# Optimization experiments

Hardware: AMD Instinct MI355X
Metric: run time of the kernel (lower is better)

Reference implementation:

```python
import jax, jax.numpy as jnp
import numpy as np

V = 1_000_000   # sparse_id_num
D = 64          # embedding_dim
F = 26          # sparse_feature_cnt
L = 8           # ids per feature bag (fixed-size ragged regularization)
B = 4096        # batch
IN_DIM = F * D  # 1664
HIDDENS = (1024, 1024, 512)


def setup_inputs() -> dict:
    key = jax.random.key(0)
    ks = jax.random.split(key, 4 + 4 * len(HIDDENS))
    inp = {}
    inp["x"] = jax.random.randint(ks[0], (B, F, L), 0, V, dtype=jnp.int64)
    inp["emb_table"] = jax.random.normal(ks[1], (V, D), dtype=jnp.float32) * 0.01
    ki = 2
    for i, h in enumerate(HIDDENS):
        inp[f"w1_{i}"] = jax.random.normal(ks[ki], (IN_DIM, h), dtype=jnp.float32) * 0.02
        inp[f"b1_{i}"] = jnp.zeros((h,), dtype=jnp.float32)
        inp[f"w2_{i}"] = jax.random.normal(ks[ki + 1], (h, IN_DIM), dtype=jnp.float32) * 0.02
        inp[f"b2_{i}"] = jnp.zeros((IN_DIM,), dtype=jnp.float32)
        ki += 2
    inp["lin_w"] = jax.random.normal(ks[ki], (IN_DIM, 1), dtype=jnp.float32) * 0.02
    inp["lin_b"] = jnp.zeros((1,), dtype=jnp.float32)
    return inp


def reference(x, emb_table,
              w1_0, b1_0, w2_0, b2_0,
              w1_1, b1_1, w2_1, b2_1,
              w1_2, b1_2, w2_2, b2_2,
              lin_w, lin_b):
    # Batched embedding lookup + sum-pool over bag dim + concat over features.
    # x: [B, F, L] -> gather [B, F, L, D] -> sum over L -> [B, F, D] -> [B, F*D]
    pooled = emb_table[x].sum(axis=2)              # [B, F, D]
    feat = pooled.reshape(x.shape[0], -1)          # [B, F*D]
    # Residual blocks: relu(linear2(relu(linear1(x))) + x)
    for w1, b1, w2, b2 in ((w1_0, b1_0, w2_0, b2_0),
                           (w1_1, b1_1, w2_1, b2_1),
                           (w1_2, b1_2, w2_2, b2_2)):
        h = jax.nn.relu(feat @ w1 + b1)
        feat = jax.nn.relu(h @ w2 + b2 + feat)
    return jax.nn.sigmoid(feat @ lin_w + lin_b)    # [B, 1]
```

## Files before the change

### kernel.cpp

```cpp
#include <hip/hip_runtime.h>

#define BATCH 4096
#define FEATS 26
#define BAG   8
#define EDIM  64
#define INDIM 1664

typedef short bf16x8 __attribute__((ext_vector_type(8)));
typedef float f32x4  __attribute__((ext_vector_type(4)));
typedef unsigned short u16x8 __attribute__((ext_vector_type(8)));

__device__ __forceinline__ unsigned short f2bf(float f) {
    unsigned u = __float_as_uint(f);
    unsigned r = (u + 0x7FFFu + ((u >> 16) & 1u)) >> 16;
    return (unsigned short)r;
}
__device__ __forceinline__ float bf2f(unsigned short h) {
    return __uint_as_float((unsigned)h << 16);
}
__device__ __forceinline__ void async_cp16(const void* g, void* lds_base_uniform) {
    __builtin_amdgcn_global_load_lds(
        (const __attribute__((address_space(1))) unsigned int*)g,
        (__attribute__((address_space(3))) unsigned int*)lds_base_uniform,
        16, 0, 0);
}
#define WAITCNT_VM(n) __builtin_amdgcn_s_waitcnt(0x0F70 | (n))

__global__ __launch_bounds__(256) void transpose_all(
    const float* __restrict__ w10, unsigned short* __restrict__ o10,
    const float* __restrict__ w20, unsigned short* __restrict__ o20,
    const float* __restrict__ w11, unsigned short* __restrict__ o11,
    const float* __restrict__ w21, unsigned short* __restrict__ o21,
    const float* __restrict__ w12, unsigned short* __restrict__ o12,
    const float* __restrict__ w22, unsigned short* __restrict__ o22)
{
    const float* in; unsigned short* out; int R, C;
    switch (blockIdx.z) {
        case 0:  in = w10; out = o10; R = INDIM; C = 1024;  break;
        case 1:  in = w20; out = o20; R = 1024;  C = INDIM; break;
        case 2:  in = w11; out = o11; R = INDIM; C = 1024;  break;
        case 3:  in = w21; out = o21; R = 1024;  C = INDIM; break;
        case 4:  in = w12; out = o12; R = INDIM; C = 512;   break;
        default: in = w22; out = o22; R = 512;   C = INDIM; break;
    }
    const int c0 = blockIdx.x * 64, r0 = blockIdx.y * 64;
    if (c0 >= C || r0 >= R) return;

    __shared__ unsigned short tile[64][65];
    const int t = threadIdx.x;
    const int tc = t & 63, tr = t >> 6;
#pragma unroll
    for (int i = 0; i < 16; ++i) {
        int r = tr + i * 4;
        tile[r][tc] = f2bf(in[(long long)(r0 + r) * C + c0 + tc]);
    }
    __syncthreads();
    const int wr = t >> 3, wc = t & 7;
#pragma unroll
    for (int half = 0; half < 2; ++half) {
        int row = wr + half * 32;
        u16x8 v;
#pragma unroll
        for (int j = 0; j < 8; ++j) v[j] = tile[wc * 8 + j][row];
        *(u16x8*)(out + (long long)(c0 + row) * R + r0 + wc * 8) = v;
    }
}

__global__ __launch_bounds__(256) void embed_pool(
    const int* __restrict__ x, const float* __restrict__ emb,
    unsigned short* __restrict__ feat)
{
    int bag  = blockIdx.x * 4 + (threadIdx.x >> 6);
    int lane = threadIdx.x & 63;
    int b = bag / FEATS;
    int f = bag - b * FEATS;
    const int* xs = x + (long long)bag * BAG;
    float s = 0.f;
#pragma unroll
    for (int l = 0; l < BAG; ++l) {
        int id = xs[l];
        s += emb[(long long)id * EDIM + lane];
    }
    feat[(long long)b * INDIM + f * EDIM + lane] = f2bf(s);
}

#define NBUF 4
__global__ __launch_bounds__(512) void gemm_bf16(
    const unsigned short* __restrict__ A, const unsigned short* __restrict__ Wt,
    const float* __restrict__ bias, const unsigned short* __restrict__ res,
    unsigned short* __restrict__ out, int M, int N, int K, int do_relu)
{
    __shared__ unsigned short As[NBUF * 128 * 32];
    __shared__ unsigned short Bs[NBUF * 128 * 32];

    const int t    = threadIdx.x;
    const int nxg = gridDim.x;
    const int lin = blockIdx.y * nxg + blockIdx.x;
    const int q   = (nxg * gridDim.y) >> 3;
    const int tile = (lin & 7) * q + (lin >> 3);
    const int ty  = tile / nxg;
    const int bCol = (tile - ty * nxg) * 128;
    const int bRow = ty * 128;

    const int wave = t >> 6, lane = t & 63;
    const int wm = wave & 1, wn = wave >> 1;
    const int lm = lane & 15, quad = lane >> 4;

    const int srow = lane >> 2;
    const int sq   = (lane & 3) ^ ((lane >> 3) & 3);
    const unsigned short* Ag = A  + (long long)(bRow + wave * 16 + srow) * K + sq * 8;
    const unsigned short* Bg = Wt + (long long)(bCol + wave * 16 + srow) * K + sq * 8;
    unsigned short* AsW = As + wave * 512;
    unsigned short* BsW = Bs + wave * 512;

    const int T = K / 32;
    f32x4 acc[4][2] = {};
    const int slot = (quad ^ ((lm >> 1) & 3)) * 8;

#define ISSUE(tile_)  do { int _b = (tile_) & (NBUF - 1);                         \
        async_cp16(Ag + (long long)(tile_) * 32, AsW + _b * 4096);                \
        async_cp16(Bg + (long long)(tile_) * 32, BsW + _b * 4096); } while (0)

#define COMPUTE(tile_) do { int _b = (tile_) & (NBUF - 1);                        \
        const unsigned short* _a = As + _b * 4096;                                \
        const unsigned short* _bp = Bs + _b * 4096;                               \
        bf16x8 af[4], bf[2];                                                      \
        _Pragma("unroll")                                                         \
        for (int i = 0; i < 4; ++i)                                               \
            af[i] = *(const bf16x8*)&_a[(wm * 64 + i * 16 + lm) * 32 + slot];     \
        _Pragma("unroll")                                                         \
        for (int j = 0; j < 2; ++j)                                               \
            bf[j] = *(const bf16x8*)&_bp[(wn * 32 + j * 16 + lm) * 32 + slot];    \
        _Pragma("unroll")                                                         \
        for (int i = 0; i < 4; ++i)                                               \
            _Pragma("unroll")                                                     \
            for (int j = 0; j < 2; ++j)                                           \
                acc[i][j] = __builtin_amdgcn_mfma_f32_16x16x32_bf16(              \
                    af[i], bf[j], acc[i][j], 0, 0, 0); } while (0)

    ISSUE(0);
    ISSUE(1);
    for (int tt = 0; tt < T - 2; ++tt) {
        ISSUE(tt + 2);
        WAITCNT_VM(4);
        asm volatile("" ::: "memory");
        __builtin_amdgcn_s_barrier();
        asm volatile("" ::: "memory");
        COMPUTE(tt);
    }
    WAITCNT_VM(2);
    asm volatile("" ::: "memory");
    __builtin_amdgcn_s_barrier();
    asm volatile("" ::: "memory");
    COMPUTE(T - 2);
    WAITCNT_VM(0);
    asm volatile("" ::: "memory");
    __builtin_amdgcn_s_barrier();
    asm volatile("" ::: "memory");
    COMPUTE(T - 1);

#pragma unroll
    for (int i = 0; i < 4; ++i) {
#pragma unroll
        for (int j = 0; j < 2; ++j) {
            int col = bCol + wn * 32 + j * 16 + lm;
            float bv = bias[col];
#pragma unroll
            for (int r = 0; r < 4; ++r) {
                int row = bRow + wm * 64 + i * 16 + quad * 4 + r;
                float v = acc[i][j][r] + bv;
                if (res) v += bf2f(res[(long long)row * N + col]);
                if (do_relu) v = fmaxf(v, 0.f);
                out[(long long)row * N + col] = f2bf(v);
            }
        }
    }
#undef ISSUE
#undef COMPUTE
}

__global__ __launch_bounds__(256) void final_head(
    const unsigned short* __restrict__ feat, const float* __restrict__ lin_w,
    const float* __restrict__ lin_b, float* __restrict__ out)
{
    int row  = blockIdx.x * 4 + (threadIdx.x >> 6);
    int lane = threadIdx.x & 63;
    const unsigned short* fr = feat + (long long)row * INDIM;
    float s = 0.f;
#pragma unroll
    for (int it = 0; it < INDIM / 64; ++it)
        s += bf2f(fr[it * 64 + lane]) * lin_w[it * 64 + lane];
#pragma unroll
    for (int off = 32; off; off >>= 1)
        s += __shfl_down(s, off, 64);
    if (lane == 0)
        out[row] = 1.f / (1.f + __expf(-(s + lin_b[0])));
}

extern "C" void kernel_launch(void* const* d_in, const int* in_sizes, int n_in,
                              void* d_out, int out_size, void* d_ws, size_t ws_size,
                              hipStream_t stream) {
    const int*   x    = (const int*)  d_in[0];
    const float* emb  = (const float*)d_in[1];
    const float* w1_0 = (const float*)d_in[2];
    const float* b1_0 = (const float*)d_in[3];
    const float* w2_0 = (const float*)d_in[4];
    const float* b2_0 = (const float*)d_in[5];
    const float* w1_1 = (const float*)d_in[6];
    const float* b1_1 = (const float*)d_in[7];
    const float* w2_1 = (const float*)d_in[8];
    const float* b2_1 = (const float*)d_in[9];
    const float* w1_2 = (const float*)d_in[10];
    const float* b1_2 = (const float*)d_in[11];
    const float* w2_2 = (const float*)d_in[12];
    const float* b2_2 = (const float*)d_in[13];
    const float* linw = (const float*)d_in[14];
    const float* linb = (const float*)d_in[15];
    float* out = (float*)d_out;

    unsigned short* feat = (unsigned short*)d_ws;
    unsigned short* h    = feat + (long long)BATCH * INDIM;
    unsigned short* p    = h + (long long)BATCH * 1024;
    unsigned short* w1_0t = p; p += 1024 * INDIM;
    unsigned short* w2_0t = p; p += INDIM * 1024;
    unsigned short* w1_1t = p; p += 1024 * INDIM;
    unsigned short* w2_1t = p; p += INDIM * 1024;
    unsigned short* w1_2t = p; p += 512 * INDIM;
    unsigned short* w2_2t = p; p += INDIM * 512;

    transpose_all<<<dim3(26, 26, 6), 256, 0, stream>>>(
        w1_0, w1_0t, w2_0, w2_0t, w1_1, w1_1t, w2_1, w2_1t, w1_2, w1_2t, w2_2, w2_2t);

    embed_pool<<<BATCH * FEATS / 4, 256, 0, stream>>>(x, emb, feat);

    gemm_bf16<<<dim3(1024/128, BATCH/128), 512, 0, stream>>>(
        feat, w1_0t, b1_0, nullptr, h, BATCH, 1024, INDIM, 1);
    gemm_bf16<<<dim3(INDIM/128, BATCH/128), 512, 0, stream>>>(
        h, w2_0t, b2_0, feat, feat, BATCH, INDIM, 1024, 1);
    gemm_bf16<<<dim3(1024/128, BATCH/128), 512, 0, stream>>>(
        feat, w1_1t, b1_1, nullptr, h, BATCH, 1024, INDIM, 1);
    gemm_bf16<<<dim3(INDIM/128, BATCH/128), 512, 0, stream>>>(
        h, w2_1t, b2_1, feat, feat, BATCH, INDIM, 1024, 1);
    gemm_bf16<<<dim3(512/128, BATCH/128), 512, 0, stream>>>(
        feat, w1_2t, b1_2, nullptr, h, BATCH, 512, INDIM, 1);
    gemm_bf16<<<dim3(INDIM/128, BATCH/128), 512, 0, stream>>>(
        h, w2_2t, b2_2, feat, feat, BATCH, INDIM, 512, 1);

    final_head<<<BATCH / 4, 256, 0, stream>>>(feat, linw, linb, out);
}
```

Before: 534.7 us.

## Deepen GEMM LDS pipeline, halve barriers, add narrow-tile GEMM and two-bag pooling

The GEMM's LDS ring buffer grows from 4 to 8 stages, and each barrier now covers two K-tiles instead of one, so the kernel synchronises half as often. The GEMM is templated on the N tile width, and the 512-wide layer uses 64-wide tiles so it launches more blocks. In that variant, waves 4-7 redundantly reload the same B rows. The embedding pooling kernel now handles two bags per wave to have more independent gathers in flight. The larger LDS footprint, about 128KB per block, likely limits occupancy to one block per CU.

Measured after the change: 553.4 us. 1.04x slower.

```diff
diff --git a/kernel.cpp b/kernel.cpp
--- a/kernel.cpp
+++ b/kernel.cpp
@@ -70,36 +70,44 @@
     const int* __restrict__ x, const float* __restrict__ emb,
     unsigned short* __restrict__ feat)
 {
-    int bag  = blockIdx.x * 4 + (threadIdx.x >> 6);
-    int lane = threadIdx.x & 63;
-    int b = bag / FEATS;
-    int f = bag - b * FEATS;
-    const int* xs = x + (long long)bag * BAG;
-    float s = 0.f;
+    const int wave = threadIdx.x >> 6, lane = threadIdx.x & 63;
+    const int bag0 = (blockIdx.x * 4 + wave) * 2;
+    const int* xs = x + (long long)bag0 * BAG;
+    float s0 = 0.f, s1 = 0.f;
 #pragma unroll
     for (int l = 0; l < BAG; ++l) {
-        int id = xs[l];
-        s += emb[(long long)id * EDIM + lane];
-    }
-    feat[(long long)b * INDIM + f * EDIM + lane] = f2bf(s);
-}
-
-#define NBUF 4
+        int id0 = xs[l];
+        int id1 = xs[BAG + l];
+        s0 += emb[(long long)id0 * EDIM + lane];
+        s1 += emb[(long long)id1 * EDIM + lane];
+    }
+#pragma unroll
+    for (int g = 0; g < 2; ++g) {
+        int bag = bag0 + g;
+        int b = bag / FEATS, f = bag - b * FEATS;
+        feat[(long long)b * INDIM + f * EDIM + lane] = f2bf(g ? s1 : s0);
+    }
+}
+
+#define NBUF 8
+template<int BN>
 __global__ __launch_bounds__(512) void gemm_bf16(
     const unsigned short* __restrict__ A, const unsigned short* __restrict__ Wt,
     const float* __restrict__ bias, const unsigned short* __restrict__ res,
     unsigned short* __restrict__ out, int M, int N, int K, int do_relu)
 {
+    constexpr int JN = BN / 64;
+
     __shared__ unsigned short As[NBUF * 128 * 32];
-    __shared__ unsigned short Bs[NBUF * 128 * 32];
-
-    const int t    = threadIdx.x;
+    __shared__ unsigned short Bs[NBUF * BN * 32];
+
+    const int t = threadIdx.x;
     const int nxg = gridDim.x;
     const int lin = blockIdx.y * nxg + blockIdx.x;
     const int q   = (nxg * gridDim.y) >> 3;
     const int tile = (lin & 7) * q + (lin >> 3);
     const int ty  = tile / nxg;
-    const int bCol = (tile - ty * nxg) * 128;
+    const int bCol = (tile - ty * nxg) * BN;
     const int bRow = ty * 128;
 
     const int wave = t >> 6, lane = t & 63;
@@ -108,62 +116,68 @@
 
     const int srow = lane >> 2;
     const int sq   = (lane & 3) ^ ((lane >> 3) & 3);
+    const int slot = (quad ^ ((lm >> 1) & 3)) * 8;
+
+    const int bwave = (BN == 128) ? wave : (wave & 3);
     const unsigned short* Ag = A  + (long long)(bRow + wave * 16 + srow) * K + sq * 8;
-    const unsigned short* Bg = Wt + (long long)(bCol + wave * 16 + srow) * K + sq * 8;
+    const unsigned short* Bg = Wt + (long long)(bCol + bwave * 16 + srow) * K + sq * 8;
     unsigned short* AsW = As + wave * 512;
-    unsigned short* BsW = Bs + wave * 512;
+    unsigned short* BsW = Bs + bwave * 512;
 
     const int T = K / 32;
-    f32x4 acc[4][2] = {};
-    const int slot = (quad ^ ((lm >> 1) & 3)) * 8;
+    const int P = T / 2;
+    f32x4 acc[4][JN] = {};
 
 #define ISSUE(tile_)  do { int _b = (tile_) & (NBUF - 1);                         \
         async_cp16(Ag + (long long)(tile_) * 32, AsW + _b * 4096);                \
-        async_cp16(Bg + (long long)(tile_) * 32, BsW + _b * 4096); } while (0)
+        async_cp16(Bg + (long long)(tile_) * 32, BsW + _b * (BN * 32)); } while (0)
 
 #define COMPUTE(tile_) do { int _b = (tile_) & (NBUF - 1);                        \
         const unsigned short* _a = As + _b * 4096;                                \
-        const unsigned short* _bp = Bs + _b * 4096;                               \
-        bf16x8 af[4], bf[2];                                                      \
+        const unsigned short* _bp = Bs + _b * (BN * 32);                          \
+        bf16x8 af[4], bf[JN];                                                     \
         _Pragma("unroll")                                                         \
         for (int i = 0; i < 4; ++i)                                               \
             af[i] = *(const bf16x8*)&_a[(wm * 64 + i * 16 + lm) * 32 + slot];     \
         _Pragma("unroll")                                                         \
-        for (int j = 0; j < 2; ++j)                                               \
-            bf[j] = *(const bf16x8*)&_bp[(wn * 32 + j * 16 + lm) * 32 + slot];    \
+        for (int j = 0; j < JN; ++j)                                              \
+            bf[j] = *(const bf16x8*)&_bp[(wn * (BN / 4) + j * 16 + lm) * 32 + slot]; \
         _Pragma("unroll")                                                         \
         for (int i = 0; i < 4; ++i)                                               \
             _Pragma("unroll")                                                     \
-            for (int j = 0; j < 2; ++j)                                           \
+            for (int j = 0; j < JN; ++j)                                          \
                 acc[i][j] = __builtin_amdgcn_mfma_f32_16x16x32_bf16(              \
                     af[i], bf[j], acc[i][j], 0, 0, 0); } while (0)
 
-    ISSUE(0);
-    ISSUE(1);
-    for (int tt = 0; tt < T - 2; ++tt) {
-        ISSUE(tt + 2);
-        WAITCNT_VM(4);
+    ISSUE(0); ISSUE(1); ISSUE(2); ISSUE(3);
+    for (int p = 0; p < P - 2; ++p) {
+        ISSUE(2 * p + 4);
+        ISSUE(2 * p + 5);
+        WAITCNT_VM(8);
         asm volatile("" ::: "memory");
         __builtin_amdgcn_s_barrier();
         asm volatile("" ::: "memory");
-        COMPUTE(tt);
-    }
-    WAITCNT_VM(2);
+        COMPUTE(2 * p);
+        COMPUTE(2 * p + 1);
+    }
+    WAITCNT_VM(4);
     asm volatile("" ::: "memory");
     __builtin_amdgcn_s_barrier();
     asm volatile("" ::: "memory");
-    COMPUTE(T - 2);
+    COMPUTE(2 * P - 4);
+    COMPUTE(2 * P - 3);
     WAITCNT_VM(0);
     asm volatile("" ::: "memory");
     __builtin_amdgcn_s_barrier();
     asm volatile("" ::: "memory");
-    COMPUTE(T - 1);
+    COMPUTE(2 * P - 2);
+    COMPUTE(2 * P - 1);
 
 #pragma unroll
     for (int i = 0; i < 4; ++i) {
 #pragma unroll
-        for (int j = 0; j < 2; ++j) {
-            int col = bCol + wn * 32 + j * 16 + lm;
+        for (int j = 0; j < JN; ++j) {
+            int col = bCol + wn * (BN / 4) + j * 16 + lm;
             float bv = bias[col];
 #pragma unroll
             for (int r = 0; r < 4; ++r) {
@@ -231,19 +245,19 @@
     transpose_all<<<dim3(26, 26, 6), 256, 0, stream>>>(
         w1_0, w1_0t, w2_0, w2_0t, w1_1, w1_1t, w2_1, w2_1t, w1_2, w1_2t, w2_2, w2_2t);
 
-    embed_pool<<<BATCH * FEATS / 4, 256, 0, stream>>>(x, emb, feat);
-
-    gemm_bf16<<<dim3(1024/128, BATCH/128), 512, 0, stream>>>(
+    embed_pool<<<BATCH * FEATS / 8, 256, 0, stream>>>(x, emb, feat);
+
+    gemm_bf16<128><<<dim3(1024/128, BATCH/128), 512, 0, stream>>>(
         feat, w1_0t, b1_0, nullptr, h, BATCH, 1024, INDIM, 1);
-    gemm_bf16<<<dim3(INDIM/128, BATCH/128), 512, 0, stream>>>(
+    gemm_bf16<128><<<dim3(INDIM/128, BATCH/128), 512, 0, stream>>>(
         h, w2_0t, b2_0, feat, feat, BATCH, INDIM, 1024, 1);
-    gemm_bf16<<<dim3(1024/128, BATCH/128), 512, 0, stream>>>(
+    gemm_bf16<128><<<dim3(1024/128, BATCH/128), 512, 0, stream>>>(
         feat, w1_1t, b1_1, nullptr, h, BATCH, 1024, INDIM, 1);
-    gemm_bf16<<<dim3(INDIM/128, BATCH/128), 512, 0, stream>>>(
+    gemm_bf16<128><<<dim3(INDIM/128, BATCH/128), 512, 0, stream>>>(
         h, w2_1t, b2_1, feat, feat, BATCH, INDIM, 1024, 1);
-    gemm_bf16<<<dim3(512/128, BATCH/128), 512, 0, stream>>>(
+    gemm_bf16<64><<<dim3(512/64, BATCH/128), 512, 0, stream>>>(
         feat, w1_2t, b1_2, nullptr, h, BATCH, 512, INDIM, 1);
-    gemm_bf16<<<dim3(INDIM/128, BATCH/128), 512, 0, stream>>>(
+    gemm_bf16<128><<<dim3(INDIM/128, BATCH/128), 512, 0, stream>>>(
         h, w2_2t, b2_2, feat, feat, BATCH, INDIM, 512, 1);
 
     final_head<<<BATCH / 4, 256, 0, stream>>>(feat, linw, linb, out);
```

## Split-K the narrow third W1 GEMM and add a reduction kernel

Applied to the files above, without the earlier changes.

The N=512 first-layer GEMM of the third residual block launches only 128 tiles, which underfills the GPU's compute units. This change splits its K dimension in two across gridDim.z, doubling the block count. Each half writes fp32 partial sums to a workspace buffer. A new reduce_split kernel then adds the two halves plus the bias, applies ReLU and writes bf16 output. The trade-off is extra fp32 partial-sum traffic and one more kernel launch, and the workspace must be large enough to hold the partials.

After: 533.3 us. No clear change (-0.3%).

```diff
diff --git a/kernel.cpp b/kernel.cpp
--- a/kernel.cpp
+++ b/kernel.cpp
@@ -88,12 +88,13 @@
 __global__ __launch_bounds__(512) void gemm_bf16(
     const unsigned short* __restrict__ A, const unsigned short* __restrict__ Wt,
     const float* __restrict__ bias, const unsigned short* __restrict__ res,
-    unsigned short* __restrict__ out, int M, int N, int K, int do_relu)
+    unsigned short* __restrict__ out, float* __restrict__ part,
+    int M, int N, int K, int do_relu)
 {
     __shared__ unsigned short As[NBUF * 128 * 32];
     __shared__ unsigned short Bs[NBUF * 128 * 32];
 
-    const int t    = threadIdx.x;
+    const int t = threadIdx.x;
     const int nxg = gridDim.x;
     const int lin = blockIdx.y * nxg + blockIdx.x;
     const int q   = (nxg * gridDim.y) >> 3;
@@ -102,18 +103,21 @@
     const int bCol = (tile - ty * nxg) * 128;
     const int bRow = ty * 128;
 
+    const int Keff = part ? (K >> 1) : K;
+    const int kOff = part ? blockIdx.z * Keff : 0;
+
     const int wave = t >> 6, lane = t & 63;
     const int wm = wave & 1, wn = wave >> 1;
     const int lm = lane & 15, quad = lane >> 4;
 
     const int srow = lane >> 2;
     const int sq   = (lane & 3) ^ ((lane >> 3) & 3);
-    const unsigned short* Ag = A  + (long long)(bRow + wave * 16 + srow) * K + sq * 8;
-    const unsigned short* Bg = Wt + (long long)(bCol + wave * 16 + srow) * K + sq * 8;
+    const unsigned short* Ag = A  + (long long)(bRow + wave * 16 + srow) * K + kOff + sq * 8;
+    const unsigned short* Bg = Wt + (long long)(bCol + wave * 16 + srow) * K + kOff + sq * 8;
     unsigned short* AsW = As + wave * 512;
     unsigned short* BsW = Bs + wave * 512;
 
-    const int T = K / 32;
+    const int T = Keff / 32;
     f32x4 acc[4][2] = {};
     const int slot = (quad ^ ((lm >> 1) & 3)) * 8;
 
@@ -159,24 +163,57 @@
     asm volatile("" ::: "memory");
     COMPUTE(T - 1);
 
-#pragma unroll
-    for (int i = 0; i < 4; ++i) {
-#pragma unroll
-        for (int j = 0; j < 2; ++j) {
-            int col = bCol + wn * 32 + j * 16 + lm;
-            float bv = bias[col];
-#pragma unroll
-            for (int r = 0; r < 4; ++r) {
-                int row = bRow + wm * 64 + i * 16 + quad * 4 + r;
-                float v = acc[i][j][r] + bv;
-                if (res) v += bf2f(res[(long long)row * N + col]);
-                if (do_relu) v = fmaxf(v, 0.f);
-                out[(long long)row * N + col] = f2bf(v);
+    if (part) {
+        float* po = part + (long long)blockIdx.z * M * N;
+#pragma unroll
+        for (int i = 0; i < 4; ++i)
+#pragma unroll
+            for (int j = 0; j < 2; ++j) {
+                int col = bCol + wn * 32 + j * 16 + lm;
+#pragma unroll
+                for (int r = 0; r < 4; ++r) {
+                    int row = bRow + wm * 64 + i * 16 + quad * 4 + r;
+                    po[(long long)row * N + col] = acc[i][j][r];
+                }
+            }
+    } else {
+#pragma unroll
+        for (int i = 0; i < 4; ++i) {
+#pragma unroll
+            for (int j = 0; j < 2; ++j) {
+                int col = bCol + wn * 32 + j * 16 + lm;
+                float bv = bias[col];
+#pragma unroll
+                for (int r = 0; r < 4; ++r) {
+                    int row = bRow + wm * 64 + i * 16 + quad * 4 + r;
+                    float v = acc[i][j][r] + bv;
+                    if (res) v += bf2f(res[(long long)row * N + col]);
+                    if (do_relu) v = fmaxf(v, 0.f);
+                    out[(long long)row * N + col] = f2bf(v);
+                }
             }
         }
     }
 #undef ISSUE
 #undef COMPUTE
+}
+
+__global__ __launch_bounds__(256) void reduce_split(
+    const float* __restrict__ part, const float* __restrict__ bias,
+    unsigned short* __restrict__ out, int M, int N)
+{
+    const long long total = (long long)M * N;
+    long long i = ((long long)blockIdx.x * 256 + threadIdx.x) * 4;
+    f32x4 a = *(const f32x4*)(part + i);
+    f32x4 b = *(const f32x4*)(part + total + i);
+    int col = (int)(i % N);
+    u16x8 dummy; (void)dummy;
+#pragma unroll
+    for (int j = 0; j < 4; ++j) {
+        float v = a[j] + b[j] + bias[col + j];
+        v = fmaxf(v, 0.f);
+        out[i + j] = f2bf(v);
+    }
 }
 
 __global__ __launch_bounds__(256) void final_head(
@@ -227,6 +264,7 @@
     unsigned short* w2_1t = p; p += INDIM * 1024;
     unsigned short* w1_2t = p; p += 512 * INDIM;
     unsigned short* w2_2t = p; p += INDIM * 512;
+    float* part = (float*)p;
 
     transpose_all<<<dim3(26, 26, 6), 256, 0, stream>>>(
         w1_0, w1_0t, w2_0, w2_0t, w1_1, w1_1t, w2_1, w2_1t, w1_2, w1_2t, w2_2, w2_2t);
@@ -234,17 +272,19 @@
     embed_pool<<<BATCH * FEATS / 4, 256, 0, stream>>>(x, emb, feat);
 
     gemm_bf16<<<dim3(1024/128, BATCH/128), 512, 0, stream>>>(
-        feat, w1_0t, b1_0, nullptr, h, BATCH, 1024, INDIM, 1);
+        feat, w1_0t, b1_0, nullptr, h, nullptr, BATCH, 1024, INDIM, 1);
     gemm_bf16<<<dim3(INDIM/128, BATCH/128), 512, 0, stream>>>(
-        h, w2_0t, b2_0, feat, feat, BATCH, INDIM, 1024, 1);
+        h, w2_0t, b2_0, feat, feat, nullptr, BATCH, INDIM, 1024, 1);
     gemm_bf16<<<dim3(1024/128, BATCH/128), 512, 0, stream>>>(
-        feat, w1_1t, b1_1, nullptr, h, BATCH, 1024, INDIM, 1);
+        feat, w1_1t, b1_1, nullptr, h, nullptr, BATCH, 1024, INDIM, 1);
     gemm_bf16<<<dim3(INDIM/128, BATCH/128), 512, 0, stream>>>(
-        h, w2_1t, b2_1, feat, feat, BATCH, INDIM, 1024, 1);
-    gemm_bf16<<<dim3(512/128, BATCH/128), 512, 0, stream>>>(
-        feat, w1_2t, b1_2, nullptr, h, BATCH, 512, INDIM, 1);
+        h, w2_1t, b2_1, feat, feat, nullptr, BATCH, INDIM, 1024, 1);
+    gemm_bf16<<<dim3(512/128, BATCH/128, 2), 512, 0, stream>>>(
+        feat, w1_2t, b1_2, nullptr, nullptr, part, BATCH, 512, INDIM, 1);
+    reduce_split<<<(BATCH * 512 / 4) / 256, 256, 0, stream>>>(
+        part, b1_2, h, BATCH, 512);
     gemm_bf16<<<dim3(INDIM/128, BATCH/128), 512, 0, stream>>>(
-        h, w2_2t, b2_2, feat, feat, BATCH, INDIM, 512, 1);
+        h, w2_2t, b2_2, feat, feat, nullptr, BATCH, INDIM, 512, 1);
 
     final_head<<<BATCH / 4, 256, 0, stream>>>(feat, linw, linb, out);
 }
```
